# Performance work log

Hardware: AMD Instinct MI355X
Metric: run time of the kernel (lower is better)

## Reference

```python
import jax, jax.numpy as jnp
import numpy as np

RC = 5.0          # radial cutoff
NB = 8            # number of Gaussian radial basis functions
NPATH = 11        # graph-conv tensor-product paths (in_way, r_way, n_contract)->out_way
NORM_FACTOR = 10.0


def setup_inputs() -> dict:
    key = jax.random.key(0)
    ks = jax.random.split(key, 24)
    N, E, C = 20000, 200000, 32
    s = 1.0 / np.sqrt(C)
    inp = {
        "rij": jax.random.normal(ks[0], (E, 3), jnp.float32) * 1.5,
        "node_x0": jax.random.normal(ks[1], (N, C), jnp.float32),
        "node_x1": jax.random.normal(ks[2], (N, C, 3), jnp.float32),
        "node_x2": jax.random.normal(ks[3], (N, C, 3, 3), jnp.float32),
        "idx_i": jax.random.randint(ks[4], (E,), 0, N, jnp.int32),
        "idx_j": jax.random.randint(ks[5], (E,), 0, N, jnp.int32),
        # radial filter MLP (rbf -> per-path per-channel filters)
        "W_rbf": jax.random.normal(ks[6], (NB, NPATH * C), jnp.float32) / np.sqrt(NB),
        "b_rbf": jax.random.normal(ks[7], (NPATH * C,), jnp.float32) * 0.1,
        # multi-body self-interaction: channel mixing per way + pair-path couplings
        "Wmix0": jax.random.normal(ks[8], (C, C), jnp.float32) * s,
        "Wmix1": jax.random.normal(ks[9], (C, C), jnp.float32) * s,
        "Wmix2": jax.random.normal(ks[10], (C, C), jnp.float32) * s,
        "coupling": jax.random.normal(ks[11], (8, C), jnp.float32) * 0.1,
        # gated nonlinearity params (gates computed from way-0 features)
        "Wg0": jax.random.normal(ks[12], (C, C), jnp.float32) * s,
        "Wg1": jax.random.normal(ks[13], (C, C), jnp.float32) * s,
        "Wg2": jax.random.normal(ks[14], (C, C), jnp.float32) * s,
        "bg0": jnp.zeros((C,), jnp.float32),
        "bg1": jnp.zeros((C,), jnp.float32),
        "bg2": jnp.zeros((C,), jnp.float32),
    }
    return inp


def _forward(rij, node_x0, node_x1, node_x2, idx_i, idx_j,
             W_rbf, b_rbf, Wmix0, Wmix1, Wmix2, coupling,
             Wg0, Wg1, Wg2, bg0, bg1, bg2):
    N, C = node_x0.shape
    # --- radial filters ---
    d = jnp.maximum(jnp.linalg.norm(rij, axis=-1), 1e-6)            # [E]
    rhat = rij / d[:, None]                                         # [E,3]
    centers = jnp.linspace(0.0, RC, NB)
    rbf = jnp.exp(-((d[:, None] - centers) ** 2) / 0.25)            # [E,NB]
    fc = 0.5 * (jnp.cos(jnp.pi * jnp.minimum(d, RC) / RC) + 1.0)    # cosine cutoff
    filt = ((rbf @ W_rbf + b_rbf) * fc[:, None]).reshape(-1, NPATH, C)  # [E,P,C]

    # --- graph conv (conv_mode='node_j'): gather neighbor tensors, tensor-product with rhat ---
    xj0 = node_x0[idx_j]                                            # [E,C]
    xj1 = node_x1[idx_j]                                            # [E,C,3]
    xj2 = node_x2[idx_j]                                            # [E,C,3,3]
    x1r = jnp.einsum('eca,ea->ec', xj1, rhat)                       # v.rhat

    m0 = filt[:, 0] * xj0
    m0 += filt[:, 5] * x1r
    m0 += filt[:, 10] * jnp.einsum('ecab,ea,eb->ec', xj2, rhat, rhat)

    m1 = jnp.einsum('ec,ea->eca', filt[:, 1] * xj0, rhat)
    m1 += filt[:, 3][:, :, None] * xj1
    m1 += jnp.einsum('ec,ea->eca', filt[:, 6] * x1r, rhat)
    m1 += filt[:, 8][:, :, None] * jnp.einsum('ecab,eb->eca', xj2, rhat)

    m2 = jnp.einsum('ec,ea,eb->ecab', filt[:, 2] * xj0, rhat, rhat)
    m2 += jnp.einsum('eca,eb->ecab', filt[:, 4][:, :, None] * xj1, rhat)
    m2 += filt[:, 7][:, :, None, None] * xj2
    m2 += filt[:, 9][:, :, None, None] * jnp.einsum('ecab,eb,ed->ecad', xj2, rhat, rhat)

    # --- scatter-add aggregation per way + normalization ---
    a0 = jax.ops.segment_sum(m0, idx_i, num_segments=N) / NORM_FACTOR
    a1 = jax.ops.segment_sum(m1, idx_i, num_segments=N) / NORM_FACTOR
    a2 = jax.ops.segment_sum(m2, idx_i, num_segments=N) / NORM_FACTOR

    # --- multi-body self-interaction (channel mix + pairwise tensor contractions) ---
    cp = coupling
    y0 = a0 @ Wmix0 \
        + cp[0] * (a0 * a0) \
        + cp[3] * jnp.einsum('nca,nca->nc', a1, a1) \
        + cp[6] * jnp.einsum('ncab,ncab->nc', a2, a2)
    y1 = jnp.einsum('nca,cd->nda', a1, Wmix1) \
        + cp[1][None, :, None] * a0[:, :, None] * a1 \
        + cp[5][None, :, None] * jnp.einsum('ncab,ncb->nca', a2, a1)
    y2 = jnp.einsum('ncab,cd->ndab', a2, Wmix2) \
        + cp[2][None, :, None, None] * a0[:, :, None, None] * a2 \
        + cp[4][None, :, None, None] * jnp.einsum('nca,ncb->ncab', a1, a1) \
        + cp[7][None, :, None, None] * jnp.einsum('ncab,ncbd->ncad', a2, a2)

    # --- gated nonlinearity (scalar channel drives gates for higher ways) ---
    z0 = jax.nn.silu(y0 @ Wg0 + bg0)
    z1 = y1 * jax.nn.silu(y0 @ Wg1 + bg1)[:, :, None]
    z2 = y2 * jax.nn.silu(y0 @ Wg2 + bg2)[:, :, None, None]

    # --- residual add (res_add) ---
    o0 = node_x0 + z0
    o1 = node_x1 + z1
    o2 = node_x2 + z2
    # pack dict {0,1,2} outputs into one array [N,C,1+3+9]
    return jnp.concatenate([o0[:, :, None], o1, o2.reshape(N, C, 9)], axis=-1)


def reference(rij, node_x0, node_x1, node_x2, idx_i, idx_j,
              W_rbf, b_rbf, Wmix0, Wmix1, Wmix2, coupling,
              Wg0, Wg1, Wg2, bg0, bg1, bg2):
    return _forward(rij, node_x0, node_x1, node_x2, idx_i, idx_j,
                    W_rbf, b_rbf, Wmix0, Wmix1, Wmix2, coupling,
                    Wg0, Wg1, Wg2, bg0, bg1, bg2)
```

## Files before the change

kernel.cpp:

```cpp
#include <hip/hip_runtime.h>
#include <cmath>

#define CH 32
#define NBASIS 8
#define NPATH 11
#define NF 13
#define NPF (NF * CH)
#define MAXDEG 40
#define NW 4

typedef unsigned int u32;
typedef __fp16 half2_t __attribute__((ext_vector_type(2)));

__device__ __forceinline__ float silu_f(float x) {
    return x / (1.0f + __expf(-x));
}

__device__ __forceinline__ u32 bf16r(float x) {
    return (__float_as_uint(x) + 0x8000u) >> 16;
}
__device__ __forceinline__ float bf16lo(u32 w) {
    return __uint_as_float(w << 16);
}
__device__ __forceinline__ float bf16hi(u32 w) {
    return __uint_as_float(w & 0xffff0000u);
}

__device__ __forceinline__ u32 f16pk(float a, float b) {
    union { half2_t h; u32 u; } cv;
    cv.h = __builtin_amdgcn_cvt_pkrtz(a, b);
    return cv.u;
}
__device__ __forceinline__ half2_t ash2(u32 w) {
    union { u32 u; half2_t h; } cv; cv.u = w; return cv.h;
}

#if __has_builtin(__builtin_amdgcn_fdot2)
__device__ __forceinline__ float dot2f(u32 a, u32 b, float c) {
    return __builtin_amdgcn_fdot2(ash2(a), ash2(b), c, false);
}
#else
__device__ __forceinline__ float dot2f(u32 a, u32 b, float c) {
    half2_t ha = ash2(a), hb = ash2(b);
    c = fmaf((float)ha.x, (float)hb.x, c);
    c = fmaf((float)ha.y, (float)hb.y, c);
    return c;
}
#endif

__device__ __forceinline__ void gload_lds16(const void* g, void* l) {
    __builtin_amdgcn_global_load_lds(
        (const __attribute__((address_space(1))) void*)g,
        (__attribute__((address_space(3))) void*)l, 16, 0, 0);
}

__global__ __launch_bounds__(256) void repack_kernel(
    const float* __restrict__ x0,
    const float* __restrict__ x1,
    const float* __restrict__ x2,
    uint4* __restrict__ xph4,
    int*   __restrict__ cnt,
    int N)
{
    int t = blockIdx.x * 256 + threadIdx.x;
    if (t < N) cnt[t] = 0;
    if (t >= N * CH) return;

    float f[13];
    f[0] = x0[t];
    const float* p1 = x1 + (size_t)t * 3;
#pragma unroll
    for (int a = 0; a < 3; a++) f[1 + a] = p1[a];
    const float* p2 = x2 + (size_t)t * 9;
#pragma unroll
    for (int q = 0; q < 9; q++) f[4 + q] = p2[q];

    u32 d[8];
#pragma unroll
    for (int qp = 0; qp < 6; qp++)
        d[qp] = bf16r(f[2 * qp]) | (bf16r(f[2 * qp + 1]) << 16);
    d[6] = bf16r(f[12]);
    d[7] = 0u;
    uint4* xo = xph4 + (size_t)t * 2;
    xo[0] = make_uint4(d[0], d[1], d[2], d[3]);
    xo[1] = make_uint4(d[4], d[5], d[6], d[7]);
}

__global__ __launch_bounds__(256) void fill_slots(
    const float* __restrict__ rij,
    const int*   __restrict__ idx_i,
    const int*   __restrict__ idx_j,
    int*    __restrict__ cnt,
    float4* __restrict__ recs,
    int E)
{
    int e = blockIdx.x * 256 + threadIdx.x;
    if (e >= E) return;

    float rx = rij[e * 3 + 0], ry = rij[e * 3 + 1], rz = rij[e * 3 + 2];
    float dn = sqrtf(rx * rx + ry * ry + rz * rz);
    float d = fmaxf(dn, 1e-6f);
    float inv = 1.0f / d;

    float rbf[NBASIS];
#pragma unroll
    for (int k = 0; k < NBASIS; k++) {
        float ck = 5.0f * (float)k / (float)(NBASIS - 1);
        float del = d - ck;
        rbf[k] = __expf(-4.0f * del * del);
    }
    float dc = fminf(d, 5.0f);
    float fc = 0.5f * (__cosf((float)M_PI * dc * 0.2f) + 1.0f);
    float scale = fc * 0.1f;

    int i = idx_i[e];
    int pos = atomicAdd(&cnt[i], 1);
    if (pos >= MAXDEG) return;

    u32 w3  = ((u32)idx_j[e] << 16) | bf16r(scale);
    u32 p01 = f16pk(rbf[0] * scale, rbf[1] * scale);
    u32 p23 = f16pk(rbf[2] * scale, rbf[3] * scale);
    u32 p45 = f16pk(rbf[4] * scale, rbf[5] * scale);
    u32 p67 = f16pk(rbf[6] * scale, rbf[7] * scale);

    float4* r = recs + 2 * (size_t)(i * MAXDEG + pos);
    r[0] = make_float4(rx * inv, ry * inv, rz * inv, __uint_as_float(w3));
    r[1] = make_float4(__uint_as_float(p01), __uint_as_float(p23),
                       __uint_as_float(p45), __uint_as_float(p67));
}

__global__ __launch_bounds__(256, 1) void edge_kernel(
    const float4*   __restrict__ recs,
    const uint4*    __restrict__ xph4,
    const int*      __restrict__ cnt,
    const float*    __restrict__ W_rbf,
    const float*    __restrict__ b_rbf,
    float* __restrict__ anode,
    int N)
{
    __shared__ uint4  sW4[NPATH * CH];
    __shared__ float4 srec[NW][MAXDEG * 2];

    int tid  = threadIdx.x;
    int wid  = tid >> 6;
    int lane = tid & 63;
    int half = lane >> 5;
    int c    = lane & 31;
    int n    = blockIdx.x * NW + wid;
    bool valid = (n < N);
    int nn = valid ? n : (N - 1);

    const char* gbase = (const char*)(recs + 2 * (size_t)nn * MAXDEG);
    {
        char* lbase = (char*)&srec[wid][0];
        gload_lds16(gbase + lane * 16, lbase);
        if (lane < 16)
            gload_lds16(gbase + 1024 + lane * 16, lbase + 1024);
    }

    const u32* recw = (const u32*)gbase;
    u32 w30 = recw[half * 8 + 3];
    u32 w31 = recw[(half + 2) * 8 + 3];
    u32 w32 = recw[(half + 4) * 8 + 3];
    int deg_g = cnt[nn];

#pragma unroll
    for (int i = 0; i < 2; i++) {
        int idx = tid + i * 256;
        if (idx < NPATH * CH) {
            int cc = idx & 31, p = idx >> 5;
            const float* w = W_rbf + p * CH + cc;
            uint4 v;
            v.x = f16pk(w[0 * NPATH * CH], w[1 * NPATH * CH]);
            v.y = f16pk(w[2 * NPATH * CH], w[3 * NPATH * CH]);
            v.z = f16pk(w[4 * NPATH * CH], w[5 * NPATH * CH]);
            v.w = f16pk(w[6 * NPATH * CH], w[7 * NPATH * CH]);
            sW4[idx] = v;
        }
    }

    float breg[NPATH];
#pragma unroll
    for (int p = 0; p < NPATH; p++) breg[p] = b_rbf[p * CH + c];

    auto gath = [&](uint4& ga, uint4& gb, u32 w3) {
        int j = (int)(w3 >> 16);
        j = j < N ? j : N - 1;
        const uint4* g = xph4 + (((size_t)j * CH + c) << 1);
        ga = g[0];
        gb = g[1];
    };

    uint4 G0a, G0b, G1a, G1b, G2a, G2b;
    gath(G0a, G0b, w30);
    gath(G1a, G1b, w31);
    gath(G2a, G2b, w32);

    __syncthreads();
    if (!valid) return;

    int deg = deg_g < MAXDEG ? deg_g : MAXDEG;

    int s0 = half, s1 = half + 2, s2 = half + 4;
    bool v0 = s0 < deg, v1 = s1 < deg, v2 = s2 < deg;

    float A0 = 0.0f, A1[3] = {0, 0, 0}, A2[9] = {0, 0, 0, 0, 0, 0, 0, 0, 0};

    const uint4* sW4c = sW4 + c;

    auto compute = [&](float4 ra, float4 rb4, uint4 ga, uint4 gb) {
        float G[13];
        G[0]  = bf16lo(ga.x); G[1]  = bf16hi(ga.x);
        G[2]  = bf16lo(ga.y); G[3]  = bf16hi(ga.y);
        G[4]  = bf16lo(ga.z); G[5]  = bf16hi(ga.z);
        G[6]  = bf16lo(ga.w); G[7]  = bf16hi(ga.w);
        G[8]  = bf16lo(gb.x); G[9]  = bf16hi(gb.x);
        G[10] = bf16lo(gb.y); G[11] = bf16hi(gb.y);
        G[12] = bf16lo(gb.z);

        float scale = bf16lo(__float_as_uint(ra.w));
        u32 pb0 = __float_as_uint(rb4.x), pb1 = __float_as_uint(rb4.y),
            pb2 = __float_as_uint(rb4.z), pb3 = __float_as_uint(rb4.w);

        float fv[NPATH];
#pragma unroll
        for (int p = 0; p < NPATH; p++) {
            uint4 wp = sW4c[p * CH];
            float acc = scale * breg[p];
            acc = dot2f(pb0, wp.x, acc);
            acc = dot2f(pb1, wp.y, acc);
            acc = dot2f(pb2, wp.z, acc);
            acc = dot2f(pb3, wp.w, acc);
            fv[p] = acc;
        }

        float hv[3] = {ra.x, ra.y, ra.z};
        float xj0 = G[0];
        float xv[3] = {G[1], G[2], G[3]};
        float x1r = xv[0] * hv[0] + xv[1] * hv[1] + xv[2] * hv[2];
        float x2r[3];
#pragma unroll
        for (int a = 0; a < 3; a++)
            x2r[a] = G[4 + a * 3 + 0] * hv[0] + G[4 + a * 3 + 1] * hv[1]
                   + G[4 + a * 3 + 2] * hv[2];
        float x2rr = x2r[0] * hv[0] + x2r[1] * hv[1] + x2r[2] * hv[2];

        A0 += fv[0] * xj0 + fv[5] * x1r + fv[10] * x2rr;

        float s01 = fv[1] * xj0 + fv[6] * x1r;
#pragma unroll
        for (int a = 0; a < 3; a++)
            A1[a] += s01 * hv[a] + fv[3] * xv[a] + fv[8] * x2r[a];

        float f2x = fv[2] * xj0;
#pragma unroll
        for (int a = 0; a < 3; a++) {
            float w = f2x * hv[a] + fv[4] * xv[a] + fv[9] * x2r[a];
#pragma unroll
            for (int b = 0; b < 3; b++)
                A2[a * 3 + b] += w * hv[b] + fv[7] * G[4 + a * 3 + b];
        }
    };

    const float4* sr = srec[wid];

    while (v0) {
        bool n0 = (s0 + 6 < deg);
        bool n1 = v1 && (s1 + 6 < deg);
        bool n2 = v2 && (s2 + 6 < deg);

        float4 ra0 = sr[2 * s0], rb0 = sr[2 * s0 + 1];
        int t0 = s0 + 6 < MAXDEG ? s0 + 6 : MAXDEG - 1;
        u32 w0n = __float_as_uint(sr[2 * t0].w);
        float4 ra1, rb1, ra2, rb2;
        u32 w1n = 0, w2n = 0;
        if (v1) {
            ra1 = sr[2 * s1]; rb1 = sr[2 * s1 + 1];
            int t1 = s1 + 6 < MAXDEG ? s1 + 6 : MAXDEG - 1;
            w1n = __float_as_uint(sr[2 * t1].w);
        }
        if (v2) {
            ra2 = sr[2 * s2]; rb2 = sr[2 * s2 + 1];
            int t2 = s2 + 6 < MAXDEG ? s2 + 6 : MAXDEG - 1;
            w2n = __float_as_uint(sr[2 * t2].w);
        }

        compute(ra0, rb0, G0a, G0b);
        if (n0) gath(G0a, G0b, w0n);
        s0 += 6; v0 = n0;

        if (v1) {
            compute(ra1, rb1, G1a, G1b);
            if (n1) gath(G1a, G1b, w1n);
            s1 += 6; v1 = n1;
        }
        if (v2) {
            compute(ra2, rb2, G2a, G2b);
            if (n2) gath(G2a, G2b, w2n);
            s2 += 6; v2 = n2;
        }
    }

    A0 += __shfl_xor(A0, 32);
#pragma unroll
    for (int a = 0; a < 3; a++) A1[a] += __shfl_xor(A1[a], 32);
#pragma unroll
    for (int q = 0; q < 9; q++) A2[q] += __shfl_xor(A2[q], 32);

    float* an = anode + (size_t)n * NPF;
    if (half == 0) {
        an[c] = A0;
#pragma unroll
        for (int a = 0; a < 3; a++) an[(1 + a) * CH + c] = A1[a];
    } else {
#pragma unroll
        for (int q = 0; q < 9; q++) an[(4 + q) * CH + c] = A2[q];
    }
}

__global__ __launch_bounds__(256) void node_update(
    const float* __restrict__ anode,
    const float* __restrict__ x0,
    const float* __restrict__ x1,
    const float* __restrict__ x2,
    const float* __restrict__ Wmix0, const float* __restrict__ Wmix1, const float* __restrict__ Wmix2,
    const float* __restrict__ coupling,
    const float* __restrict__ Wg0, const float* __restrict__ Wg1, const float* __restrict__ Wg2,
    const float* __restrict__ bg0, const float* __restrict__ bg1, const float* __restrict__ bg2,
    float* __restrict__ out, int N)
{
    __shared__ float sW[6][CH * CH];
    __shared__ float sA[8 * NPF];
    __shared__ float sy0[8][CH];
    __shared__ float ob[8 * NPF];

    int tid  = threadIdx.x;
    int nl   = tid >> 5;
    int d    = tid & 31;
    int nbase = blockIdx.x * 8;
    int n    = nbase + nl;
    int nsafe = n < N ? n : N - 1;

#pragma unroll
    for (int r = 0; r < 4; r++) {
        int idx = r * 256 + tid;
        sW[0][idx] = Wmix0[idx];
        sW[1][idx] = Wmix1[idx];
        sW[2][idx] = Wmix2[idx];
        sW[3][idx] = Wg0[idx];
        sW[4][idx] = Wg1[idx];
        sW[5][idx] = Wg2[idx];
    }
    int limit = (N - nbase) * NPF;
    if (limit > 8 * NPF) limit = 8 * NPF;
    {
        const float* ab = anode + (size_t)nbase * NPF;
#pragma unroll
        for (int r = 0; r < 13; r++) {
            int idx = r * 256 + tid;
            sA[idx] = (idx < limit) ? ab[idx] : 0.0f;
        }
    }
    __syncthreads();

    const float* An = sA + nl * NPF;

    float a0d = An[0 * CH + d];
    float a1d[3], a2d[9];
#pragma unroll
    for (int a = 0; a < 3; a++) a1d[a] = An[(1 + a) * CH + d];
#pragma unroll
    for (int q = 0; q < 9; q++) a2d[q] = An[(4 + q) * CH + d];

    float y0 = 0.0f;
#pragma unroll 8
    for (int cc = 0; cc < CH; cc++)
        y0 = fmaf(An[cc], sW[0][cc * CH + d], y0);
    {
        float cp0 = coupling[0 * CH + d], cp3 = coupling[3 * CH + d], cp6 = coupling[6 * CH + d];
        float n1v = a1d[0] * a1d[0] + a1d[1] * a1d[1] + a1d[2] * a1d[2];
        float n2v = 0.0f;
#pragma unroll
        for (int q = 0; q < 9; q++) n2v = fmaf(a2d[q], a2d[q], n2v);
        y0 += cp0 * a0d * a0d + cp3 * n1v + cp6 * n2v;
    }
    sy0[nl][d] = y0;
    __syncthreads();

    float y1[3] = {0, 0, 0};
    float y2[9] = {0, 0, 0, 0, 0, 0, 0, 0, 0};
    float g0 = bg0[d], g1 = bg1[d], g2 = bg2[d];
#pragma unroll 4
    for (int cc = 0; cc < CH; cc++) {
        float w1 = sW[1][cc * CH + d];
        float w2 = sW[2][cc * CH + d];
#pragma unroll
        for (int a = 0; a < 3; a++) y1[a] = fmaf(An[(1 + a) * CH + cc], w1, y1[a]);
#pragma unroll
        for (int q = 0; q < 9; q++) y2[q] = fmaf(An[(4 + q) * CH + cc], w2, y2[q]);
        float yv = sy0[nl][cc];
        g0 = fmaf(yv, sW[3][cc * CH + d], g0);
        g1 = fmaf(yv, sW[4][cc * CH + d], g1);
        g2 = fmaf(yv, sW[5][cc * CH + d], g2);
    }

    {
        float cp1 = coupling[1 * CH + d], cp5 = coupling[5 * CH + d];
#pragma unroll
        for (int a = 0; a < 3; a++) {
            float a2a1 = a2d[a * 3 + 0] * a1d[0] + a2d[a * 3 + 1] * a1d[1] + a2d[a * 3 + 2] * a1d[2];
            y1[a] += cp1 * a0d * a1d[a] + cp5 * a2a1;
        }
        float cp2 = coupling[2 * CH + d], cp4 = coupling[4 * CH + d], cp7 = coupling[7 * CH + d];
#pragma unroll
        for (int a = 0; a < 3; a++) {
#pragma unroll
            for (int b = 0; b < 3; b++) {
                float a2a2 = a2d[a * 3 + 0] * a2d[0 * 3 + b] + a2d[a * 3 + 1] * a2d[1 * 3 + b]
                           + a2d[a * 3 + 2] * a2d[2 * 3 + b];
                y2[a * 3 + b] += cp2 * a0d * a2d[a * 3 + b] + cp4 * a1d[a] * a1d[b] + cp7 * a2a2;
            }
        }
    }

    g0 = silu_f(g0);
    g1 = silu_f(g1);
    g2 = silu_f(g2);

    {
        const float* xs0 = x0 + (size_t)nsafe * CH;
        const float* xs1 = x1 + ((size_t)nsafe * CH + d) * 3;
        const float* xs2 = x2 + ((size_t)nsafe * CH + d) * 9;
        float* o = ob + nl * NPF + d * NF;
        o[0] = xs0[d] + g0;
#pragma unroll
        for (int a = 0; a < 3; a++)
            o[1 + a] = xs1[a] + y1[a] * g1;
#pragma unroll
        for (int q = 0; q < 9; q++)
            o[4 + q] = xs2[q] + y2[q] * g2;
    }
    __syncthreads();

    float* op = out + (size_t)nbase * NPF;
#pragma unroll
    for (int r = 0; r < 13; r++) {
        int idx = r * 256 + tid;
        if (idx < limit) op[idx] = ob[idx];
    }
}

extern "C" void kernel_launch(void* const* d_in, const int* in_sizes, int n_in,
                              void* d_out, int out_size, void* d_ws, size_t ws_size,
                              hipStream_t stream) {
    const float* rij      = (const float*)d_in[0];
    const float* x0       = (const float*)d_in[1];
    const float* x1       = (const float*)d_in[2];
    const float* x2       = (const float*)d_in[3];
    const int*   idx_i    = (const int*)d_in[4];
    const int*   idx_j    = (const int*)d_in[5];
    const float* W_rbf    = (const float*)d_in[6];
    const float* b_rbf    = (const float*)d_in[7];
    const float* Wmix0    = (const float*)d_in[8];
    const float* Wmix1    = (const float*)d_in[9];
    const float* Wmix2    = (const float*)d_in[10];
    const float* coupling = (const float*)d_in[11];
    const float* Wg0      = (const float*)d_in[12];
    const float* Wg1      = (const float*)d_in[13];
    const float* Wg2      = (const float*)d_in[14];
    const float* bg0      = (const float*)d_in[15];
    const float* bg1      = (const float*)d_in[16];
    const float* bg2      = (const float*)d_in[17];

    int E = in_sizes[4];
    int N = in_sizes[1] / CH;

    float4* recs  = (float4*)d_ws;
    uint4*  xph4  = (uint4*)(recs + 2 * (size_t)N * MAXDEG);
    int*    cnt   = (int*)(xph4 + (size_t)N * CH * 2);
    float*  anode = (float*)d_out;

    int ablocks = (N * CH + 255) / 256;
    repack_kernel<<<ablocks, 256, 0, stream>>>(x0, x1, x2, xph4, cnt, N);

    int eblocks = (E + 255) / 256;
    fill_slots<<<eblocks, 256, 0, stream>>>(rij, idx_i, idx_j, cnt, recs, E);

    edge_kernel<<<(N + NW - 1) / NW, 256, 0, stream>>>(recs, xph4, cnt,
                                                       W_rbf, b_rbf, anode, N);

    node_update<<<(N + 7) / 8, 256, 0, stream>>>(anode, x0, x1, x2,
                                                 Wmix0, Wmix1, Wmix2, coupling,
                                                 Wg0, Wg1, Wg2, bg0, bg1, bg2,
                                                 (float*)d_out, N);
}
```

Baseline: 223.7 us.

## Fuse edge aggregation with node update and merge prep kernels

Merges repack and slot-fill into one launch after a memset of the degree counters, and fuses the edge aggregation kernel with the node update so aggregated features stay in shared memory instead of going through global memory. The node update is split across the two wave halves: one half does the way-0/way-1 work and the other does way-2, and each writes its outputs straight to global memory without staging. This removes a global round-trip and launch overhead. In exchange, each block now loads the six 32x32 weight matrices for only 4 nodes, and shared memory is reused through overlapping regions.

```diff
diff --git a/kernel.cpp b/kernel.cpp
--- a/kernel.cpp
+++ b/kernel.cpp
@@ -12,6 +12,11 @@
 typedef unsigned int u32;
 typedef __fp16 half2_t __attribute__((ext_vector_type(2)));
 
+#define SM_SREC_OFF 5632
+#define SM_SA_OFF   24576
+#define SM_SY0_OFF  31232
+#define SMEM_TOTAL  31744
+
 __device__ __forceinline__ float silu_f(float x) {
     return x / (1.0f + __expf(-x));
 }
@@ -54,92 +59,101 @@
         (__attribute__((address_space(3))) void*)l, 16, 0, 0);
 }
 
-__global__ __launch_bounds__(256) void repack_kernel(
+__global__ __launch_bounds__(256) void prep_kernel(
     const float* __restrict__ x0,
     const float* __restrict__ x1,
     const float* __restrict__ x2,
     uint4* __restrict__ xph4,
-    int*   __restrict__ cnt,
-    int N)
-{
-    int t = blockIdx.x * 256 + threadIdx.x;
-    if (t < N) cnt[t] = 0;
-    if (t >= N * CH) return;
-
-    float f[13];
-    f[0] = x0[t];
-    const float* p1 = x1 + (size_t)t * 3;
-#pragma unroll
-    for (int a = 0; a < 3; a++) f[1 + a] = p1[a];
-    const float* p2 = x2 + (size_t)t * 9;
-#pragma unroll
-    for (int q = 0; q < 9; q++) f[4 + q] = p2[q];
-
-    u32 d[8];
-#pragma unroll
-    for (int qp = 0; qp < 6; qp++)
-        d[qp] = bf16r(f[2 * qp]) | (bf16r(f[2 * qp + 1]) << 16);
-    d[6] = bf16r(f[12]);
-    d[7] = 0u;
-    uint4* xo = xph4 + (size_t)t * 2;
-    xo[0] = make_uint4(d[0], d[1], d[2], d[3]);
-    xo[1] = make_uint4(d[4], d[5], d[6], d[7]);
-}
-
-__global__ __launch_bounds__(256) void fill_slots(
     const float* __restrict__ rij,
     const int*   __restrict__ idx_i,
     const int*   __restrict__ idx_j,
     int*    __restrict__ cnt,
     float4* __restrict__ recs,
-    int E)
+    int N, int E, int ablocks)
 {
-    int e = blockIdx.x * 256 + threadIdx.x;
-    if (e >= E) return;
-
-    float rx = rij[e * 3 + 0], ry = rij[e * 3 + 1], rz = rij[e * 3 + 2];
-    float dn = sqrtf(rx * rx + ry * ry + rz * rz);
-    float d = fmaxf(dn, 1e-6f);
-    float inv = 1.0f / d;
-
-    float rbf[NBASIS];
-#pragma unroll
-    for (int k = 0; k < NBASIS; k++) {
-        float ck = 5.0f * (float)k / (float)(NBASIS - 1);
-        float del = d - ck;
-        rbf[k] = __expf(-4.0f * del * del);
-    }
-    float dc = fminf(d, 5.0f);
-    float fc = 0.5f * (__cosf((float)M_PI * dc * 0.2f) + 1.0f);
-    float scale = fc * 0.1f;
-
-    int i = idx_i[e];
-    int pos = atomicAdd(&cnt[i], 1);
-    if (pos >= MAXDEG) return;
-
-    u32 w3  = ((u32)idx_j[e] << 16) | bf16r(scale);
-    u32 p01 = f16pk(rbf[0] * scale, rbf[1] * scale);
-    u32 p23 = f16pk(rbf[2] * scale, rbf[3] * scale);
-    u32 p45 = f16pk(rbf[4] * scale, rbf[5] * scale);
-    u32 p67 = f16pk(rbf[6] * scale, rbf[7] * scale);
-
-    float4* r = recs + 2 * (size_t)(i * MAXDEG + pos);
-    r[0] = make_float4(rx * inv, ry * inv, rz * inv, __uint_as_float(w3));
-    r[1] = make_float4(__uint_as_float(p01), __uint_as_float(p23),
-                       __uint_as_float(p45), __uint_as_float(p67));
-}
-
-__global__ __launch_bounds__(256, 1) void edge_kernel(
+    if ((int)blockIdx.x < ablocks) {
+        int t = blockIdx.x * 256 + threadIdx.x;
+        if (t >= N * CH) return;
+
+        float f[13];
+        f[0] = x0[t];
+        const float* p1 = x1 + (size_t)t * 3;
+#pragma unroll
+        for (int a = 0; a < 3; a++) f[1 + a] = p1[a];
+        const float* p2 = x2 + (size_t)t * 9;
+#pragma unroll
+        for (int q = 0; q < 9; q++) f[4 + q] = p2[q];
+
+        u32 d[8];
+#pragma unroll
+        for (int qp = 0; qp < 6; qp++)
+            d[qp] = bf16r(f[2 * qp]) | (bf16r(f[2 * qp + 1]) << 16);
+        d[6] = bf16r(f[12]);
+        d[7] = 0u;
+        uint4* xo = xph4 + (size_t)t * 2;
+        xo[0] = make_uint4(d[0], d[1], d[2], d[3]);
+        xo[1] = make_uint4(d[4], d[5], d[6], d[7]);
+    } else {
+        int e = ((int)blockIdx.x - ablocks) * 256 + threadIdx.x;
+        if (e >= E) return;
+
+        float rx = rij[e * 3 + 0], ry = rij[e * 3 + 1], rz = rij[e * 3 + 2];
+        float dn = sqrtf(rx * rx + ry * ry + rz * rz);
+        float d = fmaxf(dn, 1e-6f);
+        float inv = 1.0f / d;
+
+        float rbf[NBASIS];
+#pragma unroll
+        for (int k = 0; k < NBASIS; k++) {
+            float ck = 5.0f * (float)k / (float)(NBASIS - 1);
+            float del = d - ck;
+            rbf[k] = __expf(-4.0f * del * del);
+        }
+        float dc = fminf(d, 5.0f);
+        float fc = 0.5f * (__cosf((float)M_PI * dc * 0.2f) + 1.0f);
+        float scale = fc * 0.1f;
+
+        int i = idx_i[e];
+        int pos = atomicAdd(&cnt[i], 1);
+        if (pos >= MAXDEG) return;
+
+        u32 w3  = ((u32)idx_j[e] << 16) | bf16r(scale);
+        u32 p01 = f16pk(rbf[0] * scale, rbf[1] * scale);
+        u32 p23 = f16pk(rbf[2] * scale, rbf[3] * scale);
+        u32 p45 = f16pk(rbf[4] * scale, rbf[5] * scale);
+        u32 p67 = f16pk(rbf[6] * scale, rbf[7] * scale);
+
+        float4* r = recs + 2 * (size_t)(i * MAXDEG + pos);
+        r[0] = make_float4(rx * inv, ry * inv, rz * inv, __uint_as_float(w3));
+        r[1] = make_float4(__uint_as_float(p01), __uint_as_float(p23),
+                           __uint_as_float(p45), __uint_as_float(p67));
+    }
+}
+
+__global__ __launch_bounds__(256, 1) void edge_node_kernel(
     const float4*   __restrict__ recs,
     const uint4*    __restrict__ xph4,
     const int*      __restrict__ cnt,
     const float*    __restrict__ W_rbf,
     const float*    __restrict__ b_rbf,
-    float* __restrict__ anode,
-    int N)
+    const float* __restrict__ x0,
+    const float* __restrict__ x1,
+    const float* __restrict__ x2,
+    const float* __restrict__ Wmix0, const float* __restrict__ Wmix1,
+    const float* __restrict__ Wmix2,
+    const float* __restrict__ coupling,
+    const float* __restrict__ Wg0, const float* __restrict__ Wg1,
+    const float* __restrict__ Wg2,
+    const float* __restrict__ bg0, const float* __restrict__ bg1,
+    const float* __restrict__ bg2,
+    float* __restrict__ out, int N)
 {
-    __shared__ uint4  sW4[NPATH * CH];
-    __shared__ float4 srec[NW][MAXDEG * 2];
+    __shared__ __align__(16) char smem[SMEM_TOTAL];
+    uint4*  sW4  = (uint4*)smem;
+    float4* srec = (float4*)(smem + SM_SREC_OFF);
+    float*  sW6  = (float*)smem;
+    float*  sA   = (float*)(smem + SM_SA_OFF);
+    float*  sy0  = (float*)(smem + SM_SY0_OFF);
 
     int tid  = threadIdx.x;
     int wid  = tid >> 6;
@@ -152,7 +166,7 @@
 
     const char* gbase = (const char*)(recs + 2 * (size_t)nn * MAXDEG);
     {
-        char* lbase = (char*)&srec[wid][0];
+        char* lbase = (char*)(srec + (size_t)wid * (MAXDEG * 2));
         gload_lds16(gbase + lane * 16, lbase);
         if (lane < 16)
             gload_lds16(gbase + 1024 + lane * 16, lbase + 1024);
@@ -197,9 +211,8 @@
     gath(G2a, G2b, w32);
 
     __syncthreads();
-    if (!valid) return;
-
-    int deg = deg_g < MAXDEG ? deg_g : MAXDEG;
+
+    int deg = valid ? (deg_g < MAXDEG ? deg_g : MAXDEG) : 0;
 
     int s0 = half, s1 = half + 2, s2 = half + 4;
     bool v0 = s0 < deg, v1 = s1 < deg, v2 = s2 < deg;
@@ -262,7 +275,7 @@
         }
     };
 
-    const float4* sr = srec[wid];
+    const float4* sr = srec + (size_t)wid * (MAXDEG * 2);
 
     while (v0) {
         bool n0 = (s0 + 6 < deg);
@@ -307,146 +320,130 @@
 #pragma unroll
     for (int q = 0; q < 9; q++) A2[q] += __shfl_xor(A2[q], 32);
 
-    float* an = anode + (size_t)n * NPF;
-    if (half == 0) {
-        an[c] = A0;
-#pragma unroll
-        for (int a = 0; a < 3; a++) an[(1 + a) * CH + c] = A1[a];
-    } else {
-#pragma unroll
-        for (int q = 0; q < 9; q++) an[(4 + q) * CH + c] = A2[q];
-    }
-}
-
-__global__ __launch_bounds__(256) void node_update(
-    const float* __restrict__ anode,
-    const float* __restrict__ x0,
-    const float* __restrict__ x1,
-    const float* __restrict__ x2,
-    const float* __restrict__ Wmix0, const float* __restrict__ Wmix1, const float* __restrict__ Wmix2,
-    const float* __restrict__ coupling,
-    const float* __restrict__ Wg0, const float* __restrict__ Wg1, const float* __restrict__ Wg2,
-    const float* __restrict__ bg0, const float* __restrict__ bg1, const float* __restrict__ bg2,
-    float* __restrict__ out, int N)
-{
-    __shared__ float sW[6][CH * CH];
-    __shared__ float sA[8 * NPF];
-    __shared__ float sy0[8][CH];
-    __shared__ float ob[8 * NPF];
-
-    int tid  = threadIdx.x;
-    int nl   = tid >> 5;
-    int d    = tid & 31;
-    int nbase = blockIdx.x * 8;
-    int n    = nbase + nl;
-    int nsafe = n < N ? n : N - 1;
+    {
+        float* an = sA + wid * NPF;
+        if (half == 0) {
+            an[c] = A0;
+#pragma unroll
+            for (int a = 0; a < 3; a++) an[(1 + a) * CH + c] = A1[a];
+        } else {
+#pragma unroll
+            for (int q = 0; q < 9; q++) an[(4 + q) * CH + c] = A2[q];
+        }
+    }
+    __syncthreads();
 
 #pragma unroll
     for (int r = 0; r < 4; r++) {
         int idx = r * 256 + tid;
-        sW[0][idx] = Wmix0[idx];
-        sW[1][idx] = Wmix1[idx];
-        sW[2][idx] = Wmix2[idx];
-        sW[3][idx] = Wg0[idx];
-        sW[4][idx] = Wg1[idx];
-        sW[5][idx] = Wg2[idx];
-    }
-    int limit = (N - nbase) * NPF;
-    if (limit > 8 * NPF) limit = 8 * NPF;
-    {
-        const float* ab = anode + (size_t)nbase * NPF;
-#pragma unroll
-        for (int r = 0; r < 13; r++) {
-            int idx = r * 256 + tid;
-            sA[idx] = (idx < limit) ? ab[idx] : 0.0f;
-        }
+        sW6[0 * 1024 + idx] = Wmix0[idx];
+        sW6[1 * 1024 + idx] = Wmix1[idx];
+        sW6[2 * 1024 + idx] = Wmix2[idx];
+        sW6[3 * 1024 + idx] = Wg0[idx];
+        sW6[4 * 1024 + idx] = Wg1[idx];
+        sW6[5 * 1024 + idx] = Wg2[idx];
     }
     __syncthreads();
 
+    int nl = (tid >> 5) & 3;
+    int d  = tid & 31;
+    int ng = blockIdx.x * NW + nl;
+    bool phA = (tid < 128);
+    bool act = (ng < N);
     const float* An = sA + nl * NPF;
 
-    float a0d = An[0 * CH + d];
+    float a0d = An[d];
     float a1d[3], a2d[9];
 #pragma unroll
     for (int a = 0; a < 3; a++) a1d[a] = An[(1 + a) * CH + d];
 #pragma unroll
     for (int q = 0; q < 9; q++) a2d[q] = An[(4 + q) * CH + d];
 
-    float y0 = 0.0f;
+    float y2[9] = {0, 0, 0, 0, 0, 0, 0, 0, 0};
+    if (phA) {
+        float y0 = 0.0f;
 #pragma unroll 8
-    for (int cc = 0; cc < CH; cc++)
-        y0 = fmaf(An[cc], sW[0][cc * CH + d], y0);
-    {
-        float cp0 = coupling[0 * CH + d], cp3 = coupling[3 * CH + d], cp6 = coupling[6 * CH + d];
+        for (int cc = 0; cc < CH; cc++)
+            y0 = fmaf(An[cc], sW6[0 * 1024 + cc * CH + d], y0);
+        float cp0 = coupling[0 * CH + d], cp3 = coupling[3 * CH + d],
+              cp6 = coupling[6 * CH + d];
         float n1v = a1d[0] * a1d[0] + a1d[1] * a1d[1] + a1d[2] * a1d[2];
         float n2v = 0.0f;
 #pragma unroll
         for (int q = 0; q < 9; q++) n2v = fmaf(a2d[q], a2d[q], n2v);
         y0 += cp0 * a0d * a0d + cp3 * n1v + cp6 * n2v;
-    }
-    sy0[nl][d] = y0;
+        sy0[nl * CH + d] = y0;
+    } else {
+#pragma unroll 4
+        for (int cc = 0; cc < CH; cc++) {
+            float w2 = sW6[2 * 1024 + cc * CH + d];
+#pragma unroll
+            for (int q = 0; q < 9; q++)
+                y2[q] = fmaf(An[(4 + q) * CH + cc], w2, y2[q]);
+        }
+    }
     __syncthreads();
 
-    float y1[3] = {0, 0, 0};
-    float y2[9] = {0, 0, 0, 0, 0, 0, 0, 0, 0};
-    float g0 = bg0[d], g1 = bg1[d], g2 = bg2[d];
+    if (act && phA) {
+        float y1[3] = {0, 0, 0};
 #pragma unroll 4
-    for (int cc = 0; cc < CH; cc++) {
-        float w1 = sW[1][cc * CH + d];
-        float w2 = sW[2][cc * CH + d];
-#pragma unroll
-        for (int a = 0; a < 3; a++) y1[a] = fmaf(An[(1 + a) * CH + cc], w1, y1[a]);
-#pragma unroll
-        for (int q = 0; q < 9; q++) y2[q] = fmaf(An[(4 + q) * CH + cc], w2, y2[q]);
-        float yv = sy0[nl][cc];
-        g0 = fmaf(yv, sW[3][cc * CH + d], g0);
-        g1 = fmaf(yv, sW[4][cc * CH + d], g1);
-        g2 = fmaf(yv, sW[5][cc * CH + d], g2);
-    }
-
-    {
+        for (int cc = 0; cc < CH; cc++) {
+            float w1 = sW6[1 * 1024 + cc * CH + d];
+#pragma unroll
+            for (int a = 0; a < 3; a++)
+                y1[a] = fmaf(An[(1 + a) * CH + cc], w1, y1[a]);
+        }
         float cp1 = coupling[1 * CH + d], cp5 = coupling[5 * CH + d];
 #pragma unroll
         for (int a = 0; a < 3; a++) {
-            float a2a1 = a2d[a * 3 + 0] * a1d[0] + a2d[a * 3 + 1] * a1d[1] + a2d[a * 3 + 2] * a1d[2];
+            float a2a1 = a2d[a * 3 + 0] * a1d[0] + a2d[a * 3 + 1] * a1d[1]
+                       + a2d[a * 3 + 2] * a1d[2];
             y1[a] += cp1 * a0d * a1d[a] + cp5 * a2a1;
         }
-        float cp2 = coupling[2 * CH + d], cp4 = coupling[4 * CH + d], cp7 = coupling[7 * CH + d];
-#pragma unroll
-        for (int a = 0; a < 3; a++) {
-#pragma unroll
-            for (int b = 0; b < 3; b++) {
-                float a2a2 = a2d[a * 3 + 0] * a2d[0 * 3 + b] + a2d[a * 3 + 1] * a2d[1 * 3 + b]
-                           + a2d[a * 3 + 2] * a2d[2 * 3 + b];
-                y2[a * 3 + b] += cp2 * a0d * a2d[a * 3 + b] + cp4 * a1d[a] * a1d[b] + cp7 * a2a2;
-            }
-        }
-    }
-
-    g0 = silu_f(g0);
-    g1 = silu_f(g1);
-    g2 = silu_f(g2);
-
-    {
-        const float* xs0 = x0 + (size_t)nsafe * CH;
-        const float* xs1 = x1 + ((size_t)nsafe * CH + d) * 3;
-        const float* xs2 = x2 + ((size_t)nsafe * CH + d) * 9;
-        float* o = ob + nl * NPF + d * NF;
+
+        float g0 = bg0[d], g1 = bg1[d];
+#pragma unroll 8
+        for (int cc = 0; cc < CH; cc++) {
+            float yv = sy0[nl * CH + cc];
+            g0 = fmaf(yv, sW6[3 * 1024 + cc * CH + d], g0);
+            g1 = fmaf(yv, sW6[4 * 1024 + cc * CH + d], g1);
+        }
+        g0 = silu_f(g0);
+        g1 = silu_f(g1);
+
+        const float* xs0 = x0 + (size_t)ng * CH;
+        const float* xs1 = x1 + ((size_t)ng * CH + d) * 3;
+        float* o = out + (size_t)ng * NPF + d * NF;
         o[0] = xs0[d] + g0;
 #pragma unroll
         for (int a = 0; a < 3; a++)
             o[1 + a] = xs1[a] + y1[a] * g1;
+    } else if (act) {
+        float cp2 = coupling[2 * CH + d], cp4 = coupling[4 * CH + d],
+              cp7 = coupling[7 * CH + d];
+#pragma unroll
+        for (int a = 0; a < 3; a++) {
+#pragma unroll
+            for (int b = 0; b < 3; b++) {
+                float a2a2 = a2d[a * 3 + 0] * a2d[0 * 3 + b]
+                           + a2d[a * 3 + 1] * a2d[1 * 3 + b]
+                           + a2d[a * 3 + 2] * a2d[2 * 3 + b];
+                y2[a * 3 + b] += cp2 * a0d * a2d[a * 3 + b]
+                               + cp4 * a1d[a] * a1d[b] + cp7 * a2a2;
+            }
+        }
+
+        float g2 = bg2[d];
+#pragma unroll 8
+        for (int cc = 0; cc < CH; cc++)
+            g2 = fmaf(sy0[nl * CH + cc], sW6[5 * 1024 + cc * CH + d], g2);
+        g2 = silu_f(g2);
+
+        const float* xs2 = x2 + ((size_t)ng * CH + d) * 9;
+        float* o = out + (size_t)ng * NPF + d * NF;
 #pragma unroll
         for (int q = 0; q < 9; q++)
             o[4 + q] = xs2[q] + y2[q] * g2;
-    }
-    __syncthreads();
-
-    float* op = out + (size_t)nbase * NPF;
-#pragma unroll
-    for (int r = 0; r < 13; r++) {
-        int idx = r * 256 + tid;
-        if (idx < limit) op[idx] = ob[idx];
     }
 }
 
@@ -475,22 +472,19 @@
     int E = in_sizes[4];
     int N = in_sizes[1] / CH;
 
-    float4* recs  = (float4*)d_ws;
-    uint4*  xph4  = (uint4*)(recs + 2 * (size_t)N * MAXDEG);
-    int*    cnt   = (int*)(xph4 + (size_t)N * CH * 2);
-    float*  anode = (float*)d_out;
+    float4* recs = (float4*)d_ws;
+    uint4*  xph4 = (uint4*)(recs + 2 * (size_t)N * MAXDEG);
+    int*    cnt  = (int*)(xph4 + (size_t)N * CH * 2);
+
+    hipMemsetAsync(cnt, 0, (size_t)N * sizeof(int), stream);
 
     int ablocks = (N * CH + 255) / 256;
-    repack_kernel<<<ablocks, 256, 0, stream>>>(x0, x1, x2, xph4, cnt, N);
-
-    int eblocks = (E + 255) / 256;
-    fill_slots<<<eblocks, 256, 0, stream>>>(rij, idx_i, idx_j, cnt, recs, E);
-
-    edge_kernel<<<(N + NW - 1) / NW, 256, 0, stream>>>(recs, xph4, cnt,
-                                                       W_rbf, b_rbf, anode, N);
-
-    node_update<<<(N + 7) / 8, 256, 0, stream>>>(anode, x0, x1, x2,
-                                                 Wmix0, Wmix1, Wmix2, coupling,
-                                                 Wg0, Wg1, Wg2, bg0, bg1, bg2,
-                                                 (float*)d_out, N);
-}
+    int fblocks = (E + 255) / 256;
+    prep_kernel<<<ablocks + fblocks, 256, 0, stream>>>(
+        x0, x1, x2, xph4, rij, idx_i, idx_j, cnt, recs, N, E, ablocks);
+
+    edge_node_kernel<<<(N + NW - 1) / NW, 256, 0, stream>>>(
+        recs, xph4, cnt, W_rbf, b_rbf, x0, x1, x2,
+        Wmix0, Wmix1, Wmix2, coupling, Wg0, Wg1, Wg2, bg0, bg1, bg2,
+        (float*)d_out, N);
+}
```

Result: faster. 213.1 us (median of 3 runs) (-4.8%).
